# Kernel tuning notes

Measured on AMD Instinct MI355X. Metric: run time of the kernel, lower is better.

## Reference

```python
import jax, jax.numpy as jnp
import numpy as np
from jax import lax

B, OBS, E, H = 65536, 20, 64, 64


def setup_inputs() -> dict:
    key = jax.random.key(0)
    ks = jax.random.split(key, 13)
    s = 0.1
    inp = {
        "obs_traj": jax.random.normal(ks[0], (B, OBS, 2), jnp.float32),
        "W_emb": jax.random.normal(ks[1], (E, 2), jnp.float32) * s,
        "b_emb": jax.random.normal(ks[2], (E,), jnp.float32) * s,
        "Wih_e": jax.random.normal(ks[3], (4 * H, E), jnp.float32) * s,
        "Whh_e": jax.random.normal(ks[4], (4 * H, H), jnp.float32) * s,
        "bih_e": jax.random.normal(ks[5], (4 * H,), jnp.float32) * s,
        "bhh_e": jax.random.normal(ks[6], (4 * H,), jnp.float32) * s,
        "Wih_d": jax.random.normal(ks[7], (4 * H, E), jnp.float32) * s,
        "Whh_d": jax.random.normal(ks[8], (4 * H, H), jnp.float32) * s,
        "bih_d": jax.random.normal(ks[9], (4 * H,), jnp.float32) * s,
        "bhh_d": jax.random.normal(ks[10], (4 * H,), jnp.float32) * s,
        "W_fc": jax.random.normal(ks[11], (2, H), jnp.float32) * s,
        "b_fc": jax.random.normal(ks[12], (2,), jnp.float32) * s,
        "pred_len": 12,
    }
    return inp


def _lstm_step(x, h, c, Wih, Whh, b):
    # PyTorch LSTM gate order: i, f, g, o
    g = x @ Wih.T + h @ Whh.T + b  # [B, 4H]
    i, f, gg, o = jnp.split(g, 4, axis=-1)
    c2 = jax.nn.sigmoid(f) * c + jax.nn.sigmoid(i) * jnp.tanh(gg)
    h2 = jax.nn.sigmoid(o) * jnp.tanh(c2)
    return h2, c2


def reference(obs_traj, W_emb, b_emb, Wih_e, Whh_e, bih_e, bhh_e,
              Wih_d, Whh_d, bih_d, bhh_d, W_fc, b_fc, pred_len):
    bsz = obs_traj.shape[0]
    dt = obs_traj.dtype
    # Encoder: embed all observed steps at once, then scan the LSTM over time.
    emb = jax.nn.relu(obs_traj @ W_emb.T + b_emb)  # [B, OBS, E]
    b_e = bih_e + bhh_e
    h0 = jnp.zeros((bsz, H), dt)
    c0 = jnp.zeros((bsz, H), dt)

    def enc_step(carry, x_t):
        h, c = carry
        h, c = _lstm_step(x_t, h, c, Wih_e, Whh_e, b_e)
        return (h, c), None

    (h, c), _ = lax.scan(enc_step, (h0, c0), jnp.swapaxes(emb, 0, 1))

    b_d = bih_d + bhh_d
    dec_in = jax.nn.relu(obs_traj[:, -1, :] @ W_emb.T + b_emb)  # [B, E]

    def dec_step(carry, _):
        h, c, x = carry
        h, c = _lstm_step(x, h, c, Wih_d, Whh_d, b_d)
        pred = h @ W_fc.T + b_fc  # [B, 2]
        nxt = jax.nn.relu(pred @ W_emb.T + b_emb)
        return (h, c, nxt), pred

    _, preds = lax.scan(dec_step, (h, c, dec_in), None, length=pred_len)
    return jnp.swapaxes(preds, 0, 1)  # [B, pred_len, 2]
```

## Files before the change

### kernel.cpp

```cpp
#include <hip/hip_runtime.h>

typedef __bf16 bf16x8 __attribute__((ext_vector_type(8)));
typedef __bf16 bf16x4 __attribute__((ext_vector_type(4)));
typedef float  f32x4  __attribute__((ext_vector_type(4)));
typedef float  f32x2  __attribute__((ext_vector_type(2)));

constexpr int OBS   = 20;
constexpr int PRED  = 12;
constexpr int SLST  = 136;
constexpr int RPB   = 256;
constexpr int GRID  = 256;

constexpr float SIO = -1.4426950408889634f;
constexpr float SG  =  2.8853900817779268f;

constexpr int OFF_W     = 0;
constexpr int OFF_SLAB  = 65536;
constexpr int OFF_EMBC  = OFF_SLAB + 69632;
constexpr int OFF_BIASE = OFF_EMBC + 1024;
constexpr int OFF_BIASD = OFF_BIASE + 1024;
constexpr int OFF_WFC   = OFF_BIASD + 1024;
constexpr int OFF_BFC   = OFF_WFC + 512;
constexpr int LDS_BYTES = OFF_BFC + 16;

__device__ __forceinline__ float exp2_(float x) { return __builtin_amdgcn_exp2f(x); }
__device__ __forceinline__ float rcp_(float x)  { return __builtin_amdgcn_rcpf(x); }

__global__ __launch_bounds__(1024, 4)
void vanilla_lstm(const float* __restrict__ obs,
                  const float* __restrict__ W_emb, const float* __restrict__ b_emb,
                  const float* __restrict__ Wih_e, const float* __restrict__ Whh_e,
                  const float* __restrict__ bih_e, const float* __restrict__ bhh_e,
                  const float* __restrict__ Wih_d, const float* __restrict__ Whh_d,
                  const float* __restrict__ bih_d, const float* __restrict__ bhh_d,
                  const float* __restrict__ W_fc,  const float* __restrict__ b_fc,
                  float* __restrict__ out)
{
    extern __shared__ __align__(16) char lds[];
    bf16x8* wlds  = (bf16x8*)(lds + OFF_W);
    __bf16* slab  = (__bf16*)(lds + OFF_SLAB);
    float4* embc  = (float4*)(lds + OFF_EMBC);
    float*  biasE = (float*) (lds + OFF_BIASE);
    float*  biasD = (float*) (lds + OFF_BIASD);
    float*  wfc   = (float*) (lds + OFF_WFC);
    float*  bfc   = (float*) (lds + OFF_BFC);

    const int tid  = threadIdx.x;
    const int bid  = blockIdx.x;
    const int lane = tid & 63;
    const int wid  = tid >> 6;
    const int m    = lane & 15;
    const int q    = lane >> 4;
    const int srow = wid * 16 + m;
    const size_t gRowW = (size_t)bid * RPB + wid * 16;

    auto stage_W = [&](const float* Wih, const float* Whh) {
        #pragma unroll
        for (int i = 0; i < 4; ++i) {
            const int e  = tid + i * 1024;
            const int ln = e & 63;
            const int f  = e >> 6;
            const int kt = f & 3, ug = (f >> 2) & 3, c = f >> 4;
            const float sc = (c == 2) ? SG : SIO;
            const int n  = c * 64 + ug * 16 + (ln & 15);
            const int kq = (ln >> 4) * 8;
            const float* s = (kt < 2) ? (Wih + n * 64 + kt * 32 + kq)
                                      : (Whh + n * 64 + (kt - 2) * 32 + kq);
            float4 a = *(const float4*)s;
            float4 b = *(const float4*)(s + 4);
            bf16x8 v;
            v[0] = (__bf16)(sc * a.x); v[1] = (__bf16)(sc * a.y);
            v[2] = (__bf16)(sc * a.z); v[3] = (__bf16)(sc * a.w);
            v[4] = (__bf16)(sc * b.x); v[5] = (__bf16)(sc * b.y);
            v[6] = (__bf16)(sc * b.z); v[7] = (__bf16)(sc * b.w);
            wlds[f * 64 + ln] = v;
        }
    };

    stage_W(Wih_e, Whh_e);
    if (tid < 256) {
        const int ug_ = tid >> 6, c_ = (tid >> 4) & 3, u_ = tid & 15;
        const int g = c_ * 64 + ug_ * 16 + u_;
        const float sc = (c_ == 2) ? SG : SIO;
        biasE[tid] = sc * (bih_e[g] + bhh_e[g]);
        biasD[tid] = sc * (bih_d[g] + bhh_d[g]);
    }
    if (tid < 64)  embc[tid] = make_float4(W_emb[2 * tid], W_emb[2 * tid + 1], b_emb[tid], 0.f);
    if (tid < 128) wfc[tid]  = W_fc[tid];
    if (tid < 2)   bfc[tid]  = b_fc[tid];
    {
        uint4 z; z.x = z.y = z.z = z.w = 0u;
        #pragma unroll
        for (int i = 0; i < 2; ++i) {
            const int idx = tid + i * 1024;
            const int r = idx >> 3, o = idx & 7;
            *(uint4*)&slab[r * SLST + 64 + o * 8] = z;
        }
    }
    __syncthreads();

    f32x4 cst[4];
    #pragma unroll
    for (int i = 0; i < 4; ++i) cst[i] = f32x4{0.f, 0.f, 0.f, 0.f};

    auto emb_write = [&](float px0, float px1) {
        bf16x8 v0, v1;
        #pragma unroll
        for (int j = 0; j < 8; ++j) {
            float4 wc = embc[q * 16 + j];
            v0[j] = (__bf16)fmaxf(fmaf(px0, wc.x, fmaf(px1, wc.y, wc.z)), 0.f);
        }
        #pragma unroll
        for (int j = 0; j < 8; ++j) {
            float4 wc = embc[q * 16 + 8 + j];
            v1[j] = (__bf16)fmaxf(fmaf(px0, wc.x, fmaf(px1, wc.y, wc.z)), 0.f);
        }
        *(bf16x8*)&slab[srow * SLST + q * 16]     = v0;
        *(bf16x8*)&slab[srow * SLST + q * 16 + 8] = v1;
    };

    auto step = [&](const float* biasp) {
        bf16x8 B0 = *(const bf16x8*)&slab[srow * SLST +  0 + q * 8];
        bf16x8 B1 = *(const bf16x8*)&slab[srow * SLST + 32 + q * 8];
        bf16x8 B2 = *(const bf16x8*)&slab[srow * SLST + 64 + q * 8];
        bf16x8 B3 = *(const bf16x8*)&slab[srow * SLST + 96 + q * 8];
        #pragma unroll
        for (int ug = 0; ug < 4; ++ug) {
            f32x4 acc[4];
            #pragma unroll
            for (int c = 0; c < 4; ++c)
                acc[c] = *(const f32x4*)&biasp[(ug * 4 + c) * 16 + q * 4];
            #pragma unroll
            for (int c = 0; c < 4; ++c) {
                acc[c] = __builtin_amdgcn_mfma_f32_16x16x32_bf16(wlds[((c * 4 + ug) * 4 + 0) * 64 + lane], B0, acc[c], 0, 0, 0);
                acc[c] = __builtin_amdgcn_mfma_f32_16x16x32_bf16(wlds[((c * 4 + ug) * 4 + 1) * 64 + lane], B1, acc[c], 0, 0, 0);
                acc[c] = __builtin_amdgcn_mfma_f32_16x16x32_bf16(wlds[((c * 4 + ug) * 4 + 2) * 64 + lane], B2, acc[c], 0, 0, 0);
                acc[c] = __builtin_amdgcn_mfma_f32_16x16x32_bf16(wlds[((c * 4 + ug) * 4 + 3) * 64 + lane], B3, acc[c], 0, 0, 0);
            }
            f32x4 ci = cst[ug];
            bf16x4 h4;
            #pragma unroll
            for (int r = 0; r < 4; ++r) {
                const float Ef = exp2_(acc[1][r]);
                const float Ei = exp2_(acc[0][r]);
                const float Eg = exp2_(acc[2][r]);
                const float pf = 1.0f + Ef;
                const float t1 = (1.0f + Ei) * (1.0f + Eg);
                const float R  = rcp_(pf * t1);
                const float cN = fmaf(ci[r], t1, (Eg - 1.0f) * pf) * R;
                const float Eo = exp2_(acc[3][r]);
                const float Ec = exp2_(cN * SG);
                const float d2 = 1.0f + Eo;
                const float r2 = rcp_(fmaf(d2, Ec, d2));
                ci[r] = cN;
                h4[r] = (__bf16)((Ec - 1.0f) * r2);
            }
            cst[ug] = ci;
            *(bf16x4*)&slab[srow * SLST + 64 + ug * 16 + q * 4] = h4;
        }
    };

    {
        f32x2 ov = *(const f32x2*)(obs + (gRowW + m) * (OBS * 2));
        emb_write(ov[0], ov[1]);
    }
    for (int t = 0; t < OBS; ++t) {
        f32x2 ov;
        if (t + 1 < OBS) ov = *(const f32x2*)(obs + (gRowW + m) * (OBS * 2) + (t + 1) * 2);
        step(biasE);
        if (t + 1 < OBS) emb_write(ov[0], ov[1]);
    }

    __syncthreads();
    stage_W(Wih_d, Whh_d);
    __syncthreads();

    const float bfc0 = bfc[0], bfc1 = bfc[1];
    const int rr = lane >> 2, seg = lane & 3;

    for (int td = 0; td < PRED; ++td) {
        step(biasD);

        bf16x8 h0 = *(const bf16x8*)&slab[(wid * 16 + rr) * SLST + 64 + seg * 16];
        bf16x8 h1 = *(const bf16x8*)&slab[(wid * 16 + rr) * SLST + 64 + seg * 16 + 8];
        f32x4 w0 = *(const f32x4*)&wfc[seg * 16];
        f32x4 w1 = *(const f32x4*)&wfc[seg * 16 + 4];
        f32x4 w2 = *(const f32x4*)&wfc[seg * 16 + 8];
        f32x4 w3 = *(const f32x4*)&wfc[seg * 16 + 12];
        float p0 = (float)h0[0] * w0[0] + (float)h0[1] * w0[1] + (float)h0[2] * w0[2] + (float)h0[3] * w0[3]
                 + (float)h0[4] * w1[0] + (float)h0[5] * w1[1] + (float)h0[6] * w1[2] + (float)h0[7] * w1[3]
                 + (float)h1[0] * w2[0] + (float)h1[1] * w2[1] + (float)h1[2] * w2[2] + (float)h1[3] * w2[3]
                 + (float)h1[4] * w3[0] + (float)h1[5] * w3[1] + (float)h1[6] * w3[2] + (float)h1[7] * w3[3];
        f32x4 u0 = *(const f32x4*)&wfc[64 + seg * 16];
        f32x4 u1 = *(const f32x4*)&wfc[64 + seg * 16 + 4];
        f32x4 u2 = *(const f32x4*)&wfc[64 + seg * 16 + 8];
        f32x4 u3 = *(const f32x4*)&wfc[64 + seg * 16 + 12];
        float p1 = (float)h0[0] * u0[0] + (float)h0[1] * u0[1] + (float)h0[2] * u0[2] + (float)h0[3] * u0[3]
                 + (float)h0[4] * u1[0] + (float)h0[5] * u1[1] + (float)h0[6] * u1[2] + (float)h0[7] * u1[3]
                 + (float)h1[0] * u2[0] + (float)h1[1] * u2[1] + (float)h1[2] * u2[2] + (float)h1[3] * u2[3]
                 + (float)h1[4] * u3[0] + (float)h1[5] * u3[1] + (float)h1[6] * u3[2] + (float)h1[7] * u3[3];
        p0 += __shfl_xor(p0, 1, 64);  p0 += __shfl_xor(p0, 2, 64);
        p1 += __shfl_xor(p1, 1, 64);  p1 += __shfl_xor(p1, 2, 64);
        p0 += bfc0;  p1 += bfc1;
        if (seg == 0)
            *(f32x2*)&out[((gRowW + rr) * PRED + td) * 2] = f32x2{p0, p1};

        if (td + 1 < PRED) {
            float px0 = __shfl(p0, m * 4, 64);
            float px1 = __shfl(p1, m * 4, 64);
            emb_write(px0, px1);
        }
    }
}

extern "C" void kernel_launch(void* const* d_in, const int* in_sizes, int n_in,
                              void* d_out, int out_size, void* d_ws, size_t ws_size,
                              hipStream_t stream) {
    (void)in_sizes; (void)n_in; (void)d_ws; (void)ws_size; (void)out_size;
    const float* obs   = (const float*)d_in[0];
    const float* W_emb = (const float*)d_in[1];
    const float* b_emb = (const float*)d_in[2];
    const float* Wih_e = (const float*)d_in[3];
    const float* Whh_e = (const float*)d_in[4];
    const float* bih_e = (const float*)d_in[5];
    const float* bhh_e = (const float*)d_in[6];
    const float* Wih_d = (const float*)d_in[7];
    const float* Whh_d = (const float*)d_in[8];
    const float* bih_d = (const float*)d_in[9];
    const float* bhh_d = (const float*)d_in[10];
    const float* W_fc  = (const float*)d_in[11];
    const float* b_fc  = (const float*)d_in[12];
    float* o = (float*)d_out;

    static bool attr_set = false;
    if (!attr_set) {
        hipFuncSetAttribute((const void*)vanilla_lstm,
                            hipFuncAttributeMaxDynamicSharedMemorySize, LDS_BYTES);
        attr_set = true;
    }

    dim3 grid(GRID), block(1024);
    hipLaunchKernelGGL(vanilla_lstm, grid, block, LDS_BYTES, stream,
                       obs, W_emb, b_emb, Wih_e, Whh_e, bih_e, bhh_e,
                       Wih_d, Whh_d, bih_d, bhh_d, W_fc, b_fc, o);
}
```

Measured before the change: 295.3 us.

## Process two 16-row tiles per wavefront to reuse weight fragments across MFMAs

```diff
diff --git a/kernel.cpp b/kernel.cpp
--- a/kernel.cpp
+++ b/kernel.cpp
@@ -26,7 +26,7 @@
 __device__ __forceinline__ float exp2_(float x) { return __builtin_amdgcn_exp2f(x); }
 __device__ __forceinline__ float rcp_(float x)  { return __builtin_amdgcn_rcpf(x); }
 
-__global__ __launch_bounds__(1024, 4)
+__global__ __launch_bounds__(512, 2)
 void vanilla_lstm(const float* __restrict__ obs,
                   const float* __restrict__ W_emb, const float* __restrict__ b_emb,
                   const float* __restrict__ Wih_e, const float* __restrict__ Whh_e,
@@ -51,13 +51,13 @@
     const int wid  = tid >> 6;
     const int m    = lane & 15;
     const int q    = lane >> 4;
-    const int srow = wid * 16 + m;
-    const size_t gRowW = (size_t)bid * RPB + wid * 16;
+    const int wrow = wid * 32;
+    const size_t gRowW = (size_t)bid * RPB + wrow;
 
     auto stage_W = [&](const float* Wih, const float* Whh) {
         #pragma unroll
-        for (int i = 0; i < 4; ++i) {
-            const int e  = tid + i * 1024;
+        for (int i = 0; i < 8; ++i) {
+            const int e  = tid + i * 512;
             const int ln = e & 63;
             const int f  = e >> 6;
             const int kt = f & 3, ug = (f >> 2) & 3, c = f >> 4;
@@ -91,19 +91,20 @@
     {
         uint4 z; z.x = z.y = z.z = z.w = 0u;
         #pragma unroll
-        for (int i = 0; i < 2; ++i) {
-            const int idx = tid + i * 1024;
+        for (int i = 0; i < 4; ++i) {
+            const int idx = tid + i * 512;
             const int r = idx >> 3, o = idx & 7;
             *(uint4*)&slab[r * SLST + 64 + o * 8] = z;
         }
     }
     __syncthreads();
 
-    f32x4 cst[4];
+    f32x4 cst0[4], cst1[4];
     #pragma unroll
-    for (int i = 0; i < 4; ++i) cst[i] = f32x4{0.f, 0.f, 0.f, 0.f};
-
-    auto emb_write = [&](float px0, float px1) {
+    for (int i = 0; i < 4; ++i) { cst0[i] = f32x4{0.f,0.f,0.f,0.f}; cst1[i] = f32x4{0.f,0.f,0.f,0.f}; }
+
+    auto emb_write = [&](int s, float px0, float px1) {
+        const int row = wrow + s * 16 + m;
         bf16x8 v0, v1;
         #pragma unroll
         for (int j = 0; j < 8; ++j) {
@@ -115,60 +116,95 @@
             float4 wc = embc[q * 16 + 8 + j];
             v1[j] = (__bf16)fmaxf(fmaf(px0, wc.x, fmaf(px1, wc.y, wc.z)), 0.f);
         }
-        *(bf16x8*)&slab[srow * SLST + q * 16]     = v0;
-        *(bf16x8*)&slab[srow * SLST + q * 16 + 8] = v1;
+        *(bf16x8*)&slab[row * SLST + q * 16]     = v0;
+        *(bf16x8*)&slab[row * SLST + q * 16 + 8] = v1;
     };
 
     auto step = [&](const float* biasp) {
-        bf16x8 B0 = *(const bf16x8*)&slab[srow * SLST +  0 + q * 8];
-        bf16x8 B1 = *(const bf16x8*)&slab[srow * SLST + 32 + q * 8];
-        bf16x8 B2 = *(const bf16x8*)&slab[srow * SLST + 64 + q * 8];
-        bf16x8 B3 = *(const bf16x8*)&slab[srow * SLST + 96 + q * 8];
+        bf16x8 B0[4], B1[4];
+        #pragma unroll
+        for (int kt = 0; kt < 4; ++kt) {
+            B0[kt] = *(const bf16x8*)&slab[(wrow + m)      * SLST + kt * 32 + q * 8];
+            B1[kt] = *(const bf16x8*)&slab[(wrow + 16 + m) * SLST + kt * 32 + q * 8];
+        }
         #pragma unroll
         for (int ug = 0; ug < 4; ++ug) {
-            f32x4 acc[4];
-            #pragma unroll
-            for (int c = 0; c < 4; ++c)
-                acc[c] = *(const f32x4*)&biasp[(ug * 4 + c) * 16 + q * 4];
+            f32x4 a0[4], a1[4];
             #pragma unroll
             for (int c = 0; c < 4; ++c) {
-                acc[c] = __builtin_amdgcn_mfma_f32_16x16x32_bf16(wlds[((c * 4 + ug) * 4 + 0) * 64 + lane], B0, acc[c], 0, 0, 0);
-                acc[c] = __builtin_amdgcn_mfma_f32_16x16x32_bf16(wlds[((c * 4 + ug) * 4 + 1) * 64 + lane], B1, acc[c], 0, 0, 0);
-                acc[c] = __builtin_amdgcn_mfma_f32_16x16x32_bf16(wlds[((c * 4 + ug) * 4 + 2) * 64 + lane], B2, acc[c], 0, 0, 0);
-                acc[c] = __builtin_amdgcn_mfma_f32_16x16x32_bf16(wlds[((c * 4 + ug) * 4 + 3) * 64 + lane], B3, acc[c], 0, 0, 0);
-            }
-            f32x4 ci = cst[ug];
-            bf16x4 h4;
+                f32x4 b = *(const f32x4*)&biasp[(ug * 4 + c) * 16 + q * 4];
+                a0[c] = b; a1[c] = b;
+            }
             #pragma unroll
-            for (int r = 0; r < 4; ++r) {
-                const float Ef = exp2_(acc[1][r]);
-                const float Ei = exp2_(acc[0][r]);
-                const float Eg = exp2_(acc[2][r]);
-                const float pf = 1.0f + Ef;
-                const float t1 = (1.0f + Ei) * (1.0f + Eg);
-                const float R  = rcp_(pf * t1);
-                const float cN = fmaf(ci[r], t1, (Eg - 1.0f) * pf) * R;
-                const float Eo = exp2_(acc[3][r]);
-                const float Ec = exp2_(cN * SG);
-                const float d2 = 1.0f + Eo;
-                const float r2 = rcp_(fmaf(d2, Ec, d2));
-                ci[r] = cN;
-                h4[r] = (__bf16)((Ec - 1.0f) * r2);
-            }
-            cst[ug] = ci;
-            *(bf16x4*)&slab[srow * SLST + 64 + ug * 16 + q * 4] = h4;
+            for (int kt = 0; kt < 4; ++kt) {
+                #pragma unroll
+                for (int c = 0; c < 4; ++c) {
+                    bf16x8 w = wlds[((c * 4 + ug) * 4 + kt) * 64 + lane];
+                    a0[c] = __builtin_amdgcn_mfma_f32_16x16x32_bf16(w, B0[kt], a0[c], 0, 0, 0);
+                    a1[c] = __builtin_amdgcn_mfma_f32_16x16x32_bf16(w, B1[kt], a1[c], 0, 0, 0);
+                }
+            }
+            {
+                f32x4 ci = cst0[ug];
+                bf16x4 h4;
+                #pragma unroll
+                for (int r = 0; r < 4; ++r) {
+                    const float Ef = exp2_(a0[1][r]);
+                    const float Ei = exp2_(a0[0][r]);
+                    const float Eg = exp2_(a0[2][r]);
+                    const float pf = 1.0f + Ef;
+                    const float t1 = (1.0f + Ei) * (1.0f + Eg);
+                    const float R  = rcp_(pf * t1);
+                    const float cN = fmaf(ci[r], t1, (Eg - 1.0f) * pf) * R;
+                    const float Eo = exp2_(a0[3][r]);
+                    const float Ec = exp2_(cN * SG);
+                    const float d2 = 1.0f + Eo;
+                    const float r2 = rcp_(fmaf(d2, Ec, d2));
+                    ci[r] = cN;
+                    h4[r] = (__bf16)((Ec - 1.0f) * r2);
+                }
+                cst0[ug] = ci;
+                *(bf16x4*)&slab[(wrow + m) * SLST + 64 + ug * 16 + q * 4] = h4;
+            }
+            {
+                f32x4 ci = cst1[ug];
+                bf16x4 h4;
+                #pragma unroll
+                for (int r = 0; r < 4; ++r) {
+                    const float Ef = exp2_(a1[1][r]);
+                    const float Ei = exp2_(a1[0][r]);
+                    const float Eg = exp2_(a1[2][r]);
+                    const float pf = 1.0f + Ef;
+                    const float t1 = (1.0f + Ei) * (1.0f + Eg);
+                    const float R  = rcp_(pf * t1);
+                    const float cN = fmaf(ci[r], t1, (Eg - 1.0f) * pf) * R;
+                    const float Eo = exp2_(a1[3][r]);
+                    const float Ec = exp2_(cN * SG);
+                    const float d2 = 1.0f + Eo;
+                    const float r2 = rcp_(fmaf(d2, Ec, d2));
+                    ci[r] = cN;
+                    h4[r] = (__bf16)((Ec - 1.0f) * r2);
+                }
+                cst1[ug] = ci;
+                *(bf16x4*)&slab[(wrow + 16 + m) * SLST + 64 + ug * 16 + q * 4] = h4;
+            }
         }
     };
 
     {
-        f32x2 ov = *(const f32x2*)(obs + (gRowW + m) * (OBS * 2));
-        emb_write(ov[0], ov[1]);
+        f32x2 o0 = *(const f32x2*)(obs + (gRowW + m)      * (OBS * 2));
+        f32x2 o1 = *(const f32x2*)(obs + (gRowW + 16 + m) * (OBS * 2));
+        emb_write(0, o0[0], o0[1]);
+        emb_write(1, o1[0], o1[1]);
     }
     for (int t = 0; t < OBS; ++t) {
-        f32x2 ov;
-        if (t + 1 < OBS) ov = *(const f32x2*)(obs + (gRowW + m) * (OBS * 2) + (t + 1) * 2);
+        f32x2 o0, o1;
+        if (t + 1 < OBS) {
+            o0 = *(const f32x2*)(obs + (gRowW + m)      * (OBS * 2) + (t + 1) * 2);
+            o1 = *(const f32x2*)(obs + (gRowW + 16 + m) * (OBS * 2) + (t + 1) * 2);
+        }
         step(biasE);
-        if (t + 1 < OBS) emb_write(ov[0], ov[1]);
+        if (t + 1 < OBS) { emb_write(0, o0[0], o0[1]); emb_write(1, o1[0], o1[1]); }
     }
 
     __syncthreads();
@@ -181,34 +217,38 @@
     for (int td = 0; td < PRED; ++td) {
         step(biasD);
 
-        bf16x8 h0 = *(const bf16x8*)&slab[(wid * 16 + rr) * SLST + 64 + seg * 16];
-        bf16x8 h1 = *(const bf16x8*)&slab[(wid * 16 + rr) * SLST + 64 + seg * 16 + 8];
-        f32x4 w0 = *(const f32x4*)&wfc[seg * 16];
-        f32x4 w1 = *(const f32x4*)&wfc[seg * 16 + 4];
-        f32x4 w2 = *(const f32x4*)&wfc[seg * 16 + 8];
-        f32x4 w3 = *(const f32x4*)&wfc[seg * 16 + 12];
-        float p0 = (float)h0[0] * w0[0] + (float)h0[1] * w0[1] + (float)h0[2] * w0[2] + (float)h0[3] * w0[3]
-                 + (float)h0[4] * w1[0] + (float)h0[5] * w1[1] + (float)h0[6] * w1[2] + (float)h0[7] * w1[3]
-                 + (float)h1[0] * w2[0] + (float)h1[1] * w2[1] + (float)h1[2] * w2[2] + (float)h1[3] * w2[3]
-                 + (float)h1[4] * w3[0] + (float)h1[5] * w3[1] + (float)h1[6] * w3[2] + (float)h1[7] * w3[3];
-        f32x4 u0 = *(const f32x4*)&wfc[64 + seg * 16];
-        f32x4 u1 = *(const f32x4*)&wfc[64 + seg * 16 + 4];
-        f32x4 u2 = *(const f32x4*)&wfc[64 + seg * 16 + 8];
-        f32x4 u3 = *(const f32x4*)&wfc[64 + seg * 16 + 12];
-        float p1 = (float)h0[0] * u0[0] + (float)h0[1] * u0[1] + (float)h0[2] * u0[2] + (float)h0[3] * u0[3]
-                 + (float)h0[4] * u1[0] + (float)h0[5] * u1[1] + (float)h0[6] * u1[2] + (float)h0[7] * u1[3]
-                 + (float)h1[0] * u2[0] + (float)h1[1] * u2[1] + (float)h1[2] * u2[2] + (float)h1[3] * u2[3]
-                 + (float)h1[4] * u3[0] + (float)h1[5] * u3[1] + (float)h1[6] * u3[2] + (float)h1[7] * u3[3];
-        p0 += __shfl_xor(p0, 1, 64);  p0 += __shfl_xor(p0, 2, 64);
-        p1 += __shfl_xor(p1, 1, 64);  p1 += __shfl_xor(p1, 2, 64);
-        p0 += bfc0;  p1 += bfc1;
-        if (seg == 0)
-            *(f32x2*)&out[((gRowW + rr) * PRED + td) * 2] = f32x2{p0, p1};
-
-        if (td + 1 < PRED) {
-            float px0 = __shfl(p0, m * 4, 64);
-            float px1 = __shfl(p1, m * 4, 64);
-            emb_write(px0, px1);
+        #pragma unroll
+        for (int s = 0; s < 2; ++s) {
+            const int hrow = wrow + s * 16 + rr;
+            bf16x8 h0 = *(const bf16x8*)&slab[hrow * SLST + 64 + seg * 16];
+            bf16x8 h1 = *(const bf16x8*)&slab[hrow * SLST + 64 + seg * 16 + 8];
+            f32x4 w0 = *(const f32x4*)&wfc[seg * 16];
+            f32x4 w1 = *(const f32x4*)&wfc[seg * 16 + 4];
+            f32x4 w2 = *(const f32x4*)&wfc[seg * 16 + 8];
+            f32x4 w3 = *(const f32x4*)&wfc[seg * 16 + 12];
+            float p0 = (float)h0[0] * w0[0] + (float)h0[1] * w0[1] + (float)h0[2] * w0[2] + (float)h0[3] * w0[3]
+                     + (float)h0[4] * w1[0] + (float)h0[5] * w1[1] + (float)h0[6] * w1[2] + (float)h0[7] * w1[3]
+                     + (float)h1[0] * w2[0] + (float)h1[1] * w2[1] + (float)h1[2] * w2[2] + (float)h1[3] * w2[3]
+                     + (float)h1[4] * w3[0] + (float)h1[5] * w3[1] + (float)h1[6] * w3[2] + (float)h1[7] * w3[3];
+            f32x4 u0 = *(const f32x4*)&wfc[64 + seg * 16];
+            f32x4 u1 = *(const f32x4*)&wfc[64 + seg * 16 + 4];
+            f32x4 u2 = *(const f32x4*)&wfc[64 + seg * 16 + 8];
+            f32x4 u3 = *(const f32x4*)&wfc[64 + seg * 16 + 12];
+            float p1 = (float)h0[0] * u0[0] + (float)h0[1] * u0[1] + (float)h0[2] * u0[2] + (float)h0[3] * u0[3]
+                     + (float)h0[4] * u1[0] + (float)h0[5] * u1[1] + (float)h0[6] * u1[2] + (float)h0[7] * u1[3]
+                     + (float)h1[0] * u2[0] + (float)h1[1] * u2[1] + (float)h1[2] * u2[2] + (float)h1[3] * u2[3]
+                     + (float)h1[4] * u3[0] + (float)h1[5] * u3[1] + (float)h1[6] * u3[2] + (float)h1[7] * u3[3];
+            p0 += __shfl_xor(p0, 1, 64);  p0 += __shfl_xor(p0, 2, 64);
+            p1 += __shfl_xor(p1, 1, 64);  p1 += __shfl_xor(p1, 2, 64);
+            p0 += bfc0;  p1 += bfc1;
+            if (seg == 0)
+                *(f32x2*)&out[((gRowW + s * 16 + rr) * PRED + td) * 2] = f32x2{p0, p1};
+
+            if (td + 1 < PRED) {
+                float px0 = __shfl(p0, m * 4, 64);
+                float px1 = __shfl(p1, m * 4, 64);
+                emb_write(s, px0, px1);
+            }
         }
     }
 }
@@ -239,7 +279,7 @@
         attr_set = true;
     }
 
-    dim3 grid(GRID), block(1024);
+    dim3 grid(GRID), block(512);
     hipLaunchKernelGGL(vanilla_lstm, grid, block, LDS_BYTES, stream,
                        obs, W_emb, b_emb, Wih_e, Whh_e, bih_e, bhh_e,
                        Wih_d, Whh_d, bih_d, bhh_d, W_fc, b_fc, o);
```

After: 295.8 us. About the same (+0.2%).
